# Kernel tuning notes

Hardware: AMD Instinct MI355X
Metric: run time of the kernel (lower is better)

The kernel has to match this reference:

```python
import jax, jax.numpy as jnp
import numpy as np

B, T, C, H = 8, 2048, 768, 64

def setup_inputs() -> dict:
    key = jax.random.key(0)
    k1, k2, k3, k4 = jax.random.split(key, 4)
    x = jax.random.normal(k1, (B, T, C), dtype=jnp.float32)
    Wk = jax.random.normal(k2, (C, H), dtype=jnp.float32) * 0.02
    Wq = jax.random.normal(k3, (C, H), dtype=jnp.float32) * 0.02
    Wv = jax.random.normal(k4, (C, H), dtype=jnp.float32) * 0.02
    return {"x": x, "Wk": Wk, "Wq": Wq, "Wv": Wv}

def reference(x, Wk, Wq, Wv):
    # QKV projections (no bias): [B,T,C] @ [C,H] -> [B,T,H]
    k = jnp.einsum('btc,ch->bth', x, Wk)
    q = jnp.einsum('btc,ch->bth', x, Wq)
    v = jnp.einsum('btc,ch->bth', x, Wv)
    scale = 1.0 / jnp.sqrt(jnp.asarray(q.shape[-1], q.dtype))
    # scores: [B,T,T]
    wei = jnp.einsum('bth,bsh->bts', q, k) * scale
    # causal mask: upper triangle (k=1) set to -inf before softmax
    causal = jnp.tril(jnp.ones((wei.shape[1], wei.shape[2]), dtype=bool))
    wei = jnp.where(causal[None, :, :], wei, -jnp.inf)
    wei = jax.nn.softmax(wei, axis=-1)
    # dropout deterministic (training=False) -> identity
    out = jnp.einsum('bts,bsh->bth', wei, v)
    return out
```

## Files before the change

### kernel.cpp

```cpp
#include <hip/hip_runtime.h>
#include <hip/hip_bf16.h>
#include <stdint.h>

#define BB 8
#define TT 2048
#define CC 768
#define NTPB 72

typedef __bf16 bf16x8 __attribute__((ext_vector_type(8)));
typedef float f32x4 __attribute__((ext_vector_type(4)));
typedef float f32x16 __attribute__((ext_vector_type(16)));

__device__ inline __bf16 f2b(float f) {
    __hip_bfloat16 h = __float2bfloat16(f);
    return __builtin_bit_cast(__bf16, h);
}
__device__ inline ushort f2bits(float f) {
    __hip_bfloat16 h = __float2bfloat16(f);
    return __builtin_bit_cast(ushort, h);
}
__device__ inline uint32_t cvtpk(float lo, float hi) {
    uint32_t r;
    asm("v_cvt_pk_bf16_f32 %0, %1, %2" : "=v"(r) : "v"(lo), "v"(hi));
    return r;
}
__device__ inline void pswap(uint32_t& a, uint32_t& b) {
    asm volatile("v_permlane32_swap_b32 %0, %1" : "+v"(a), "+v"(b));
}

#define GLL16(gp, lp)                                                          \
    __builtin_amdgcn_global_load_lds(                                          \
        (const __attribute__((address_space(1))) unsigned int*)(gp),           \
        (__attribute__((address_space(3))) unsigned int*)(lp), 16, 0, 0)

__launch_bounds__(256)
__global__ void wt_kernel(const float* __restrict__ Wk, const float* __restrict__ Wq,
                          const float* __restrict__ Wv, ushort* __restrict__ WtF) {
    __shared__ float tile[64][65];
    int m  = blockIdx.x / 12;
    int c0 = (blockIdx.x % 12) * 64;
    const float* W = (m == 0) ? Wq : ((m == 1) ? Wk : Wv);
    int tid = threadIdx.x;
#pragma unroll
    for (int i = 0; i < 4; i++) {
        int r   = (tid >> 4) + i * 16;
        int col = (tid & 15) * 4;
        float4 v = *(const float4*)&W[(size_t)(c0 + r) * 64 + col];
        tile[r][col] = v.x; tile[r][col + 1] = v.y;
        tile[r][col + 2] = v.z; tile[r][col + 3] = v.w;
    }
    __syncthreads();
    int j  = tid >> 2;
    int cc = (tid & 3) * 16;
    ushort tmp[16];
#pragma unroll
    for (int e = 0; e < 16; e++) tmp[e] = f2bits(tile[cc + e][j]);
    int c  = m * 64 + j;
    int kb = c0 + cc;
    int kc = kb >> 5;
    int h4 = (kb >> 3) & 3;
    ushort* dst = &WtF[((size_t)kc * 192 + c) * 32 + h4 * 8];
    *(uint4*)(dst)     = *(uint4*)&tmp[0];
    *(uint4*)(dst + 8) = *(uint4*)&tmp[8];
}

__launch_bounds__(256, 2)
__global__ void qkv_kernel(const float* __restrict__ x, const ushort* __restrict__ WtF,
                           ushort* __restrict__ qws, ushort* __restrict__ kws,
                           ushort* __restrict__ vws) {
    __shared__ float  xsA[4][32 * 32];
    __shared__ ushort xsB[4][6144];

    int tid  = threadIdx.x;
    int wid  = tid >> 6;
    int lane = tid & 63;
    int l15  = lane & 15;
    int hi4  = lane >> 4;
    int row0 = blockIdx.x * 32;

    int rA  = tid >> 3;
    int gcA = (tid & 7) ^ (rA & 7);
    const float* gpA = x + (size_t)(row0 + rA) * CC + gcA * 4;

    int PB0 = tid, PB1 = tid + 256, PB2 = tid + 512;
    int LB0 = PB0 ^ ((PB0 >> 3) & 3);
    int LB1 = PB1 ^ ((PB1 >> 3) & 3);
    int LB2 = PB2 ^ ((PB2 >> 3) & 3);

    int PrB[3];
#pragma unroll
    for (int nt = 0; nt < 3; nt++) {
        int Lr = (wid * 48 + nt * 16 + l15) * 4 + hi4;
        PrB[nt] = Lr ^ ((Lr >> 3) & 3);
    }

    f32x4 acc[2][3];
#pragma unroll
    for (int mm = 0; mm < 2; mm++)
#pragma unroll
        for (int nt = 0; nt < 3; nt++) acc[mm][nt] = (f32x4){0.f, 0.f, 0.f, 0.f};

    auto stage = [&](int t) {
        int buf = t & 3;
        GLL16(gpA + t * 32, &xsA[buf][(size_t)tid * 4]);
        const ushort* bsrc = WtF + (size_t)t * 6144;
        GLL16(bsrc + LB0 * 8, &xsB[buf][PB0 * 8]);
        GLL16(bsrc + LB1 * 8, &xsB[buf][PB1 * 8]);
        GLL16(bsrc + LB2 * 8, &xsB[buf][PB2 * 8]);
    };

    stage(0); stage(1); stage(2); stage(3);

#pragma unroll
    for (int t = 0; t < 24; t++) {
        if (t <= 20)      asm volatile("s_waitcnt vmcnt(12)" ::: "memory");
        else if (t == 21) asm volatile("s_waitcnt vmcnt(8)" ::: "memory");
        else if (t == 22) asm volatile("s_waitcnt vmcnt(4)" ::: "memory");
        else              asm volatile("s_waitcnt vmcnt(0)" ::: "memory");
        __builtin_amdgcn_s_barrier();
        __builtin_amdgcn_sched_barrier(0);

        int buf = t & 3;
        bf16x8 af[2];
#pragma unroll
        for (int mm = 0; mm < 2; mm++) {
            int row = mm * 16 + l15;
            const float* base = &xsA[buf][row * 32];
            float4 fa = *(const float4*)(base + (((2 * hi4)     ^ (row & 7)) * 4));
            float4 fb = *(const float4*)(base + (((2 * hi4 + 1) ^ (row & 7)) * 4));
            uint32_t w0 = cvtpk(fa.x, fa.y), w1 = cvtpk(fa.z, fa.w);
            uint32_t w2 = cvtpk(fb.x, fb.y), w3 = cvtpk(fb.z, fb.w);
            uint4 u = {w0, w1, w2, w3};
            af[mm] = __builtin_bit_cast(bf16x8, u);
        }
#pragma unroll
        for (int nt = 0; nt < 3; nt++) {
            bf16x8 b = __builtin_bit_cast(bf16x8, *(const uint4*)&xsB[buf][PrB[nt] * 8]);
            acc[0][nt] = __builtin_amdgcn_mfma_f32_16x16x32_bf16(af[0], b, acc[0][nt], 0, 0, 0);
            acc[1][nt] = __builtin_amdgcn_mfma_f32_16x16x32_bf16(af[1], b, acc[1][nt], 0, 0, 0);
        }
        __builtin_amdgcn_s_barrier();
        if (t + 4 < 24) stage(t + 4);
    }

    int bidx = row0 >> 11;
#pragma unroll
    for (int mm = 0; mm < 2; mm++) {
        int r0 = row0 + mm * 16 + 4 * hi4;
        int t0 = r0 & 2047;
#pragma unroll
        for (int nt = 0; nt < 3; nt++) {
            int c = wid * 48 + nt * 16 + l15;
            int m = c >> 6;
            int j = c & 63;
            if (m == 0) {
#pragma unroll
                for (int r = 0; r < 4; r++)
                    qws[(size_t)(r0 + r) * 64 + j] = f2bits(acc[mm][nt][r] * 0.125f);
            } else if (m == 1) {
#pragma unroll
                for (int r = 0; r < 4; r++)
                    kws[(size_t)(r0 + r) * 64 + j] = f2bits(acc[mm][nt][r]);
            } else {
                ushort4 pk;
                pk.x = f2bits(acc[mm][nt][0]);
                pk.y = f2bits(acc[mm][nt][1]);
                pk.z = f2bits(acc[mm][nt][2]);
                pk.w = f2bits(acc[mm][nt][3]);
                *(ushort4*)&vws[((size_t)bidx * 64 + j) * TT + t0] = pk;
            }
        }
    }
}

__launch_bounds__(256, 3)
__global__ void flash_kernel(const ushort* __restrict__ qg, const ushort* __restrict__ kg,
                             const ushort* __restrict__ vtg, float* __restrict__ out,
                             float* __restrict__ pO, float* __restrict__ pM,
                             float* __restrict__ pL) {
    __shared__ ushort Ks[3][64 * 64];
    __shared__ ushort Vs[3][64 * 64];

    int tid  = threadIdx.x;
    int wid  = tid >> 6;
    int lane = tid & 63;
    int l31  = lane & 31;
    int hi   = lane >> 5;

    int b  = blockIdx.x / NTPB;
    int tp = blockIdx.x - b * NTPB;
    int g  = 0;
    while (tp >= ((g + 2) * (g + 2)) >> 2) g++;
    int seg   = tp - (((g + 1) * (g + 1)) >> 2);
    int nseg  = (g + 2) >> 1;
    int Qb    = g * 128;
    int Q0w   = Qb + wid * 32;
    int s_beg = seg * 256;
    int s_end = (s_beg + 256 < Qb + 128) ? s_beg + 256 : Qb + 128;
    int nt    = (s_end - s_beg) >> 6;

    int rS  = tid >> 3;
    int gcS = (tid & 7) ^ (rS & 7);
    const ushort* kS = kg  + ((size_t)b * TT + rS) * 64 + gcS * 8;
    const ushort* vS = vtg + ((size_t)b * 64 + rS) * TT + gcS * 8;

    auto stage = [&](int tt) {
        int buf = tt % 3;
        int ss  = s_beg + tt * 64;
        const ushort* kA = kS + (size_t)ss * 64;
        const ushort* vA = vS + ss;
        GLL16(kA,            &Ks[buf][tid * 8]);
        GLL16(kA + 32 * 64,  &Ks[buf][(tid + 256) * 8]);
        GLL16(vA,            &Vs[buf][tid * 8]);
        GLL16(vA + 32 * TT,  &Vs[buf][(tid + 256) * 8]);
    };

    const ushort* qp = qg + ((size_t)b * TT + Q0w + l31) * 64 + hi * 8;
    bf16x8 qf[4];
#pragma unroll
    for (int c = 0; c < 4; c++)
        qf[c] = __builtin_bit_cast(bf16x8, *(const uint4*)(qp + c * 16));

    f32x16 o0 = (f32x16)(0.f), o1 = (f32x16)(0.f);
    float m  = -INFINITY;
    float lp = 0.f;

    stage(0);
    if (nt > 1) stage(1);

    for (int t = 0; t < nt; t++) {
        if (t < nt - 1) asm volatile("s_waitcnt vmcnt(4)" ::: "memory");
        else            asm volatile("s_waitcnt vmcnt(0)" ::: "memory");
        __builtin_amdgcn_s_barrier();
        __builtin_amdgcn_sched_barrier(0);
        if (t + 2 < nt) stage(t + 2);

        int s0 = s_beg + t * 64;
        if (s0 < Q0w + 32) {
            int buf = t % 3;
            bf16x8 kf[2][4];
#pragma unroll
            for (int tt = 0; tt < 2; tt++) {
                int rk = tt * 32 + l31;
                const ushort* base = &Ks[buf][rk * 64];
                int sw = rk & 7;
#pragma unroll
                for (int c = 0; c < 4; c++)
                    kf[tt][c] = __builtin_bit_cast(bf16x8,
                        *(const uint4*)(base + (((c * 2 + hi) ^ sw) * 8)));
            }

            f32x16 st0 = (f32x16)(0.f), st1 = (f32x16)(0.f);
            __builtin_amdgcn_s_setprio(1);
#pragma unroll
            for (int c = 0; c < 4; c++)
                st0 = __builtin_amdgcn_mfma_f32_32x32x16_bf16(kf[0][c], qf[c], st0, 0, 0, 0);
#pragma unroll
            for (int c = 0; c < 4; c++)
                st1 = __builtin_amdgcn_mfma_f32_32x32x16_bf16(kf[1][c], qf[c], st1, 0, 0, 0);
            __builtin_amdgcn_s_setprio(0);

            if (s0 + 63 > Q0w) {
                int th0 = Q0w + l31 - s0 - 4 * hi;
                int th1 = th0 - 32;
#pragma unroll
                for (int r = 0; r < 16; r++) {
                    int kvl = (r & 3) + 8 * (r >> 2);
                    if (kvl > th0) st0[r] = -INFINITY;
                    if (kvl > th1) st1[r] = -INFINITY;
                }
            }

            float lmax = -INFINITY;
#pragma unroll
            for (int r = 0; r < 16; r++) lmax = fmaxf(lmax, fmaxf(st0[r], st1[r]));
            float pmax = fmaxf(lmax, __shfl_xor(lmax, 32));
            if (__any(pmax > m + 8.f)) {
                float mn = fmaxf(m, pmax);
                float al = __expf(m - mn);
                lp *= al;
#pragma unroll
                for (int r = 0; r < 16; r++) { o0[r] *= al; o1[r] *= al; }
                m = mn;
            }
#pragma unroll
            for (int r = 0; r < 16; r++) {
                st0[r] = __expf(st0[r] - m); lp += st0[r];
                st1[r] = __expf(st1[r] - m); lp += st1[r];
            }

            bf16x8 pf[4];
            {
                uint32_t w0, w1, w2, w3;
                w0 = cvtpk(st0[0], st0[1]);  w1 = cvtpk(st0[2], st0[3]);
                w2 = cvtpk(st0[4], st0[5]);  w3 = cvtpk(st0[6], st0[7]);
                pswap(w0, w2); pswap(w1, w3);
                uint4 u0 = {w0, w1, w2, w3}; pf[0] = __builtin_bit_cast(bf16x8, u0);
                w0 = cvtpk(st0[8], st0[9]);  w1 = cvtpk(st0[10], st0[11]);
                w2 = cvtpk(st0[12], st0[13]); w3 = cvtpk(st0[14], st0[15]);
                pswap(w0, w2); pswap(w1, w3);
                uint4 u1 = {w0, w1, w2, w3}; pf[1] = __builtin_bit_cast(bf16x8, u1);
                w0 = cvtpk(st1[0], st1[1]);  w1 = cvtpk(st1[2], st1[3]);
                w2 = cvtpk(st1[4], st1[5]);  w3 = cvtpk(st1[6], st1[7]);
                pswap(w0, w2); pswap(w1, w3);
                uint4 u2 = {w0, w1, w2, w3}; pf[2] = __builtin_bit_cast(bf16x8, u2);
                w0 = cvtpk(st1[8], st1[9]);  w1 = cvtpk(st1[10], st1[11]);
                w2 = cvtpk(st1[12], st1[13]); w3 = cvtpk(st1[14], st1[15]);
                pswap(w0, w2); pswap(w1, w3);
                uint4 u3 = {w0, w1, w2, w3}; pf[3] = __builtin_bit_cast(bf16x8, u3);
            }

            bf16x8 vf[2][4];
#pragma unroll
            for (int ht = 0; ht < 2; ht++) {
                int rv = ht * 32 + l31;
                const ushort* base = &Vs[buf][rv * 64];
                int sw = rv & 7;
#pragma unroll
                for (int c = 0; c < 4; c++)
                    vf[ht][c] = __builtin_bit_cast(bf16x8,
                        *(const uint4*)(base + (((c * 2 + hi) ^ sw) * 8)));
            }

            __builtin_amdgcn_s_setprio(1);
#pragma unroll
            for (int c = 0; c < 4; c++)
                o0 = __builtin_amdgcn_mfma_f32_32x32x16_bf16(vf[0][c], pf[c], o0, 0, 0, 0);
#pragma unroll
            for (int c = 0; c < 4; c++)
                o1 = __builtin_amdgcn_mfma_f32_32x32x16_bf16(vf[1][c], pf[c], o1, 0, 0, 0);
            __builtin_amdgcn_s_setprio(0);
        }
    }

    float lsum = lp + __shfl_xor(lp, 32);

    if (nseg == 1) {
        float inv = 1.f / lsum;
        float* ob = out + ((size_t)b * TT + Q0w + l31) * 64;
#pragma unroll
        for (int gg = 0; gg < 4; gg++) {
            float4 v0 = {o0[4*gg] * inv, o0[4*gg+1] * inv, o0[4*gg+2] * inv, o0[4*gg+3] * inv};
            *(float4*)(ob + 8 * gg + 4 * hi) = v0;
            float4 v1 = {o1[4*gg] * inv, o1[4*gg+1] * inv, o1[4*gg+2] * inv, o1[4*gg+3] * inv};
            *(float4*)(ob + 32 + 8 * gg + 4 * hi) = v1;
        }
    } else {
        int tb = b * NTPB + tp;
        float* pb = pO + (size_t)tb * 8192 + (size_t)(wid * 32 + l31) * 64;
#pragma unroll
        for (int gg = 0; gg < 4; gg++) {
            float4 v0 = {o0[4*gg], o0[4*gg+1], o0[4*gg+2], o0[4*gg+3]};
            *(float4*)(pb + 8 * gg + 4 * hi) = v0;
            float4 v1 = {o1[4*gg], o1[4*gg+1], o1[4*gg+2], o1[4*gg+3]};
            *(float4*)(pb + 32 + 8 * gg + 4 * hi) = v1;
        }
        if (hi == 0) {
            pM[(size_t)tb * 128 + wid * 32 + l31] = m;
            pL[(size_t)tb * 128 + wid * 32 + l31] = lsum;
        }
    }
}

__launch_bounds__(256)
__global__ void merge_kernel(const float* __restrict__ pO, const float* __restrict__ pM,
                             const float* __restrict__ pL, float* __restrict__ out) {
    int b    = blockIdx.x / 14;
    int g    = 2 + (blockIdx.x % 14);
    int nseg = (g + 2) >> 1;
    int tbase = b * NTPB + (((g + 1) * (g + 1)) >> 2);

    int row = threadIdx.x >> 1;
    int hh  = (threadIdx.x & 1) * 32;

    float mstar = -INFINITY;
    for (int s = 0; s < nseg; s++)
        mstar = fmaxf(mstar, pM[(size_t)(tbase + s) * 128 + row]);

    float oa[32];
#pragma unroll
    for (int i = 0; i < 32; i++) oa[i] = 0.f;
    float la = 0.f;
    for (int s = 0; s < nseg; s++) {
        float w = __expf(pM[(size_t)(tbase + s) * 128 + row] - mstar);
        la += w * pL[(size_t)(tbase + s) * 128 + row];
        const float* pp = pO + (size_t)(tbase + s) * 8192 + (size_t)row * 64 + hh;
#pragma unroll
        for (int i = 0; i < 8; i++) {
            float4 v = *(const float4*)(pp + i * 4);
            oa[i*4]   += w * v.x; oa[i*4+1] += w * v.y;
            oa[i*4+2] += w * v.z; oa[i*4+3] += w * v.w;
        }
    }
    float inv = 1.f / la;
    float* ob = out + ((size_t)b * TT + g * 128 + row) * 64 + hh;
#pragma unroll
    for (int i = 0; i < 8; i++) {
        float4 v = {oa[i*4] * inv, oa[i*4+1] * inv, oa[i*4+2] * inv, oa[i*4+3] * inv};
        *(float4*)(ob + i * 4) = v;
    }
}

extern "C" void kernel_launch(void* const* d_in, const int* in_sizes, int n_in,
                              void* d_out, int out_size, void* d_ws, size_t ws_size,
                              hipStream_t stream) {
    const float* x  = (const float*)d_in[0];
    const float* Wk = (const float*)d_in[1];
    const float* Wq = (const float*)d_in[2];
    const float* Wv = (const float*)d_in[3];
    float* out = (float*)d_out;

    char* ws = (char*)d_ws;
    ushort* WtF = (ushort*)(ws);
    ushort* qws = (ushort*)(ws + 0x50000);
    ushort* kws = (ushort*)(ws + 0x250000);
    ushort* vws = (ushort*)(ws + 0x450000);
    float*  pO  = (float*)(ws + 0x650000);
    float*  pM  = (float*)(ws + 0x1850000);
    float*  pL  = (float*)(ws + 0x1898000);

    wt_kernel<<<36, 256, 0, stream>>>(Wk, Wq, Wv, WtF);
    qkv_kernel<<<(BB * TT) / 32, 256, 0, stream>>>(x, WtF, qws, kws, vws);
    flash_kernel<<<BB * NTPB, 256, 0, stream>>>(qws, kws, vws, out, pO, pM, pL);
    merge_kernel<<<BB * 14, 256, 0, stream>>>(pO, pM, pL, out);
}
```

Baseline: 55.01 us.

## Deepen KV pipeline, use exp2 softmax, tree reductions, and bf16 partial outputs

New measurement: 56.56 us. +2.8%, slower.

```diff
diff --git a/kernel.cpp b/kernel.cpp
--- a/kernel.cpp
+++ b/kernel.cpp
@@ -18,6 +18,9 @@
 __device__ inline ushort f2bits(float f) {
     __hip_bfloat16 h = __float2bfloat16(f);
     return __builtin_bit_cast(ushort, h);
+}
+__device__ inline float bits2f(ushort u) {
+    return __builtin_bit_cast(float, ((uint32_t)u) << 16);
 }
 __device__ inline uint32_t cvtpk(float lo, float hi) {
     uint32_t r;
@@ -143,6 +146,7 @@
         if (t + 4 < 24) stage(t + 4);
     }
 
+    const float qscale = 0.125f * 1.4426950408889634f;
     int bidx = row0 >> 11;
 #pragma unroll
     for (int mm = 0; mm < 2; mm++) {
@@ -156,7 +160,7 @@
             if (m == 0) {
 #pragma unroll
                 for (int r = 0; r < 4; r++)
-                    qws[(size_t)(r0 + r) * 64 + j] = f2bits(acc[mm][nt][r] * 0.125f);
+                    qws[(size_t)(r0 + r) * 64 + j] = f2bits(acc[mm][nt][r] * qscale);
             } else if (m == 1) {
 #pragma unroll
                 for (int r = 0; r < 4; r++)
@@ -173,13 +177,13 @@
     }
 }
 
-__launch_bounds__(256, 3)
+__launch_bounds__(256, 2)
 __global__ void flash_kernel(const ushort* __restrict__ qg, const ushort* __restrict__ kg,
                              const ushort* __restrict__ vtg, float* __restrict__ out,
-                             float* __restrict__ pO, float* __restrict__ pM,
+                             ushort* __restrict__ pO, float* __restrict__ pM,
                              float* __restrict__ pL) {
-    __shared__ ushort Ks[3][64 * 64];
-    __shared__ ushort Vs[3][64 * 64];
+    __shared__ ushort Ks[4][64 * 64];
+    __shared__ ushort Vs[4][64 * 64];
 
     int tid  = threadIdx.x;
     int wid  = tid >> 6;
@@ -205,7 +209,7 @@
     const ushort* vS = vtg + ((size_t)b * 64 + rS) * TT + gcS * 8;
 
     auto stage = [&](int tt) {
-        int buf = tt % 3;
+        int buf = tt & 3;
         int ss  = s_beg + tt * 64;
         const ushort* kA = kS + (size_t)ss * 64;
         const ushort* vA = vS + ss;
@@ -227,17 +231,20 @@
 
     stage(0);
     if (nt > 1) stage(1);
+    if (nt > 2) stage(2);
 
     for (int t = 0; t < nt; t++) {
-        if (t < nt - 1) asm volatile("s_waitcnt vmcnt(4)" ::: "memory");
-        else            asm volatile("s_waitcnt vmcnt(0)" ::: "memory");
+        int ahead = nt - 1 - t;
+        if (ahead >= 2)      asm volatile("s_waitcnt vmcnt(8)" ::: "memory");
+        else if (ahead == 1) asm volatile("s_waitcnt vmcnt(4)" ::: "memory");
+        else                 asm volatile("s_waitcnt vmcnt(0)" ::: "memory");
         __builtin_amdgcn_s_barrier();
         __builtin_amdgcn_sched_barrier(0);
-        if (t + 2 < nt) stage(t + 2);
+        if (t + 3 < nt) stage(t + 3);
 
         int s0 = s_beg + t * 64;
         if (s0 < Q0w + 32) {
-            int buf = t % 3;
+            int buf = t & 3;
             bf16x8 kf[2][4];
 #pragma unroll
             for (int tt = 0; tt < 2; tt++) {
@@ -271,13 +278,18 @@
                 }
             }
 
-            float lmax = -INFINITY;
-#pragma unroll
-            for (int r = 0; r < 16; r++) lmax = fmaxf(lmax, fmaxf(st0[r], st1[r]));
-            float pmax = fmaxf(lmax, __shfl_xor(lmax, 32));
-            if (__any(pmax > m + 8.f)) {
+            float a[16];
+#pragma unroll
+            for (int r = 0; r < 16; r++) a[r] = fmaxf(st0[r], st1[r]);
+#pragma unroll
+            for (int off = 8; off > 0; off >>= 1)
+#pragma unroll
+                for (int i = 0; i < 8; i++)
+                    if (i < off) a[i] = fmaxf(a[i], a[i + off]);
+            float pmax = fmaxf(a[0], __shfl_xor(a[0], 32));
+            if (__any(pmax > m + 11.54f)) {
                 float mn = fmaxf(m, pmax);
-                float al = __expf(m - mn);
+                float al = exp2f(m - mn);
                 lp *= al;
 #pragma unroll
                 for (int r = 0; r < 16; r++) { o0[r] *= al; o1[r] *= al; }
@@ -285,9 +297,18 @@
             }
 #pragma unroll
             for (int r = 0; r < 16; r++) {
-                st0[r] = __expf(st0[r] - m); lp += st0[r];
-                st1[r] = __expf(st1[r] - m); lp += st1[r];
-            }
+                st0[r] = exp2f(st0[r] - m);
+                st1[r] = exp2f(st1[r] - m);
+            }
+            float s[16];
+#pragma unroll
+            for (int r = 0; r < 16; r++) s[r] = st0[r] + st1[r];
+#pragma unroll
+            for (int off = 8; off > 0; off >>= 1)
+#pragma unroll
+                for (int i = 0; i < 8; i++)
+                    if (i < off) s[i] += s[i + off];
+            lp += s[0];
 
             bf16x8 pf[4];
             {
@@ -347,13 +368,15 @@
         }
     } else {
         int tb = b * NTPB + tp;
-        float* pb = pO + (size_t)tb * 8192 + (size_t)(wid * 32 + l31) * 64;
+        ushort* pb = pO + (size_t)tb * 8192 + (size_t)(wid * 32 + l31) * 64;
 #pragma unroll
         for (int gg = 0; gg < 4; gg++) {
-            float4 v0 = {o0[4*gg], o0[4*gg+1], o0[4*gg+2], o0[4*gg+3]};
-            *(float4*)(pb + 8 * gg + 4 * hi) = v0;
-            float4 v1 = {o1[4*gg], o1[4*gg+1], o1[4*gg+2], o1[4*gg+3]};
-            *(float4*)(pb + 32 + 8 * gg + 4 * hi) = v1;
+            ushort4 v0 = {f2bits(o0[4*gg]), f2bits(o0[4*gg+1]),
+                          f2bits(o0[4*gg+2]), f2bits(o0[4*gg+3])};
+            *(ushort4*)(pb + 8 * gg + 4 * hi) = v0;
+            ushort4 v1 = {f2bits(o1[4*gg]), f2bits(o1[4*gg+1]),
+                          f2bits(o1[4*gg+2]), f2bits(o1[4*gg+3])};
+            *(ushort4*)(pb + 32 + 8 * gg + 4 * hi) = v1;
         }
         if (hi == 0) {
             pM[(size_t)tb * 128 + wid * 32 + l31] = m;
@@ -363,7 +386,7 @@
 }
 
 __launch_bounds__(256)
-__global__ void merge_kernel(const float* __restrict__ pO, const float* __restrict__ pM,
+__global__ void merge_kernel(const ushort* __restrict__ pO, const float* __restrict__ pM,
                              const float* __restrict__ pL, float* __restrict__ out) {
     int b    = blockIdx.x / 14;
     int g    = 2 + (blockIdx.x % 14);
@@ -382,14 +405,22 @@
     for (int i = 0; i < 32; i++) oa[i] = 0.f;
     float la = 0.f;
     for (int s = 0; s < nseg; s++) {
-        float w = __expf(pM[(size_t)(tbase + s) * 128 + row] - mstar);
+        float w = exp2f(pM[(size_t)(tbase + s) * 128 + row] - mstar);
         la += w * pL[(size_t)(tbase + s) * 128 + row];
-        const float* pp = pO + (size_t)(tbase + s) * 8192 + (size_t)row * 64 + hh;
-#pragma unroll
-        for (int i = 0; i < 8; i++) {
-            float4 v = *(const float4*)(pp + i * 4);
-            oa[i*4]   += w * v.x; oa[i*4+1] += w * v.y;
-            oa[i*4+2] += w * v.z; oa[i*4+3] += w * v.w;
+        const ushort* pp = pO + (size_t)(tbase + s) * 8192 + (size_t)row * 64 + hh;
+        uint4 u0 = *(const uint4*)(pp);
+        uint4 u1 = *(const uint4*)(pp + 8);
+        uint4 u2 = *(const uint4*)(pp + 16);
+        uint4 u3 = *(const uint4*)(pp + 24);
+        const uint4 uu[4] = {u0, u1, u2, u3};
+#pragma unroll
+        for (int q = 0; q < 4; q++) {
+#pragma unroll
+            for (int e = 0; e < 4; e++) {
+                uint32_t wdw = ((const uint32_t*)&uu[q])[e];
+                oa[q*8 + e*2]     += w * bits2f((ushort)(wdw & 0xffff));
+                oa[q*8 + e*2 + 1] += w * bits2f((ushort)(wdw >> 16));
+            }
         }
     }
     float inv = 1.f / la;
@@ -415,9 +446,9 @@
     ushort* qws = (ushort*)(ws + 0x50000);
     ushort* kws = (ushort*)(ws + 0x250000);
     ushort* vws = (ushort*)(ws + 0x450000);
-    float*  pO  = (float*)(ws + 0x650000);
-    float*  pM  = (float*)(ws + 0x1850000);
-    float*  pL  = (float*)(ws + 0x1898000);
+    ushort* pO  = (ushort*)(ws + 0x650000);
+    float*  pM  = (float*)(ws + 0x1050000);
+    float*  pL  = (float*)(ws + 0x1098000);
 
     wt_kernel<<<36, 256, 0, stream>>>(Wk, Wq, Wv, WtF);
     qkv_kernel<<<(BB * TT) / 32, 256, 0, stream>>>(x, WtF, qws, kws, vws);
```
